# Performance work log

Measured on AMD Instinct MI355X. Metric: run time of the kernel, lower is better.

The kernel has to match this reference:

```python
import jax, jax.numpy as jnp
import numpy as np

N_NODES = 100_000
N_EDGES = 1_600_000
N_GRAPHS = 256          # num_segments for batch scatter (static)
T_CAPS = 16             # num_target_cap
IN_CH = 64
OUT_CH = 64
NUM_ROUTES = 3
BN_EPS = 1e-5


def squash(s, axis=-1):
    # v = (|s|^2 / (1+|s|^2)) * s / |s|
    sq = jnp.sum(s * s, axis=axis, keepdims=True)
    return (sq / (1.0 + sq)) * s / jnp.sqrt(sq + 1e-16)


def setup_inputs() -> dict:
    key = jax.random.key(0)
    k_x, k_ei, k_ew, k_b, k_w, k_bias = jax.random.split(key, 6)
    x = jax.random.normal(k_x, (N_NODES, IN_CH), dtype=jnp.float32)
    edge_index = jax.random.randint(k_ei, (2, N_EDGES), 0, N_NODES, dtype=jnp.int32)
    edge_weight = jax.random.uniform(k_ew, (N_EDGES,), dtype=jnp.float32)
    batch = jnp.sort(jax.random.randint(k_b, (N_NODES,), 0, N_GRAPHS, dtype=jnp.int32))
    # per-capsule GCNConv weights, stacked: (T, in, out), bias (T, out)
    W = jax.random.normal(k_w, (T_CAPS, IN_CH, OUT_CH), dtype=jnp.float32) * 0.05
    bias = jax.random.normal(k_bias, (T_CAPS, OUT_CH), dtype=jnp.float32) * 0.05
    bn_gamma = jnp.ones((IN_CH,), dtype=jnp.float32)
    bn_beta = jnp.zeros((IN_CH,), dtype=jnp.float32)
    return {"x": x, "edge_index": edge_index, "edge_weight": edge_weight,
            "batch": batch, "bn_gamma": bn_gamma, "bn_beta": bn_beta,
            "W": W, "bias": bias}


def reference(x, edge_index, edge_weight, batch, bn_gamma, bn_beta, W, bias):
    N = x.shape[0]
    T = W.shape[0]
    # --- BatchNorm1d (training-mode batch statistics, biased variance) ---
    mu = jnp.mean(x, axis=0)
    var = jnp.var(x, axis=0)
    xn = (x - mu) * jax.lax.rsqrt(var + BN_EPS) * bn_gamma + bn_beta

    # --- GCNConv (shared graph): A_hat x, then per-capsule linear ---
    row, col = edge_index[0], edge_index[1]
    ar = jnp.arange(N, dtype=edge_index.dtype)
    row_f = jnp.concatenate([row, ar])              # add self-loops, weight 1
    col_f = jnp.concatenate([col, ar])
    w_f = jnp.concatenate([edge_weight, jnp.ones((N,), x.dtype)])
    deg = jax.ops.segment_sum(w_f, col_f, num_segments=N)
    dinv = jnp.where(deg > 0, jax.lax.rsqrt(deg), 0.0)
    norm = dinv[row_f] * w_f * dinv[col_f]          # (E+N,)
    h = jax.ops.segment_sum(norm[:, None] * xn[row_f], col_f, num_segments=N)  # (N, in)
    # linearity: propagate(A, x W_t) == (propagate(A, x)) W_t
    u_hat = jnp.einsum('ni,tio->nto', h, W) + bias[None]  # (N, T, D)

    # --- dynamic routing ---
    node_deg = jax.ops.segment_sum(edge_weight, row, num_segments=N)  # (N,)
    b_log = jnp.broadcast_to(node_deg[:, None, None], (N, T, 1))
    u_det = jax.lax.stop_gradient(u_hat)
    for _ in range(NUM_ROUTES - 1):
        c = jax.nn.softmax(b_log, axis=1)                         # (N, T, 1)
        s = jax.ops.segment_sum(c * u_det, batch, num_segments=N_GRAPHS)  # (G, T, D)
        v = squash(s, axis=-1)
        vg = v[batch]                                             # (N, T, D)
        b_log = b_log + jnp.sum(u_det * vg, axis=-1, keepdims=True)
    c = jax.nn.softmax(b_log, axis=1)
    s = jax.ops.segment_sum(c * u_hat, batch, num_segments=N_GRAPHS)  # (G, T, D)

    # --- add per-graph mean of (normalized) node features ---
    cnt = jax.ops.segment_sum(jnp.ones((N,), x.dtype), batch, num_segments=N_GRAPHS)
    x_mean = jax.ops.segment_sum(xn, batch, num_segments=N_GRAPHS) / jnp.maximum(cnt, 1.0)[:, None]
    s = s + x_mean[:, None, :]                                    # needs in==out
    v = squash(s, axis=-1)

    # --- final_layer=True: v.norm(p=-1, dim=-1) = (sum |v|^-1)^-1 ---
    out = 1.0 / jnp.sum(1.0 / jnp.abs(v), axis=-1)                # (G, T)
    return out
```

## Files before the change

kernel.cpp:

```cpp
#include <hip/hip_runtime.h>
#include <hip/hip_fp16.h>
#include <math.h>

#define N_NODES 100000
#define N_EDGES 1600000
#define N_GRAPHS 256
#define T_CAPS 16
#define D_CH 64
#define BN_EPS 1e-5f
#define NSPLIT 8
#define CHUNK 32
#define FIX_SCALE 33554432.0f
#define NB 782
#define EPB 4096
#define NBLK 391
#define NBN 512

__device__ __forceinline__ float waveReduceSum(float v) {
    for (int m = 32; m >= 1; m >>= 1) v += __shfl_xor(v, m, 64);
    return v;
}

__global__ void setup_kernel(float* bn_sums, float* hsum, float* xsum,
                             const float* __restrict__ W, float* __restrict__ WT,
                             const int* __restrict__ batch, int* __restrict__ gstart) {
    int idx = blockIdx.x * blockDim.x + threadIdx.x;
    if (idx < 128) bn_sums[idx] = 0.0f;
    if (idx < N_GRAPHS * D_CH) { hsum[idx] = 0.0f; xsum[idx] = 0.0f; }
    if (idx < T_CAPS * 64 * 64) {
        int t = idx >> 12, rem = idx & 4095, o = rem >> 6, i = rem & 63;
        WT[idx] = W[t * 4096 + i * 64 + o];
    }
    if (idx <= N_GRAPHS) {
        int lo = 0, hi = N_NODES;
        while (lo < hi) { int mid = (lo + hi) >> 1; if (batch[mid] < idx) lo = mid + 1; else hi = mid; }
        gstart[idx] = lo;
    }
}

__global__ void passA_bn_kernel(const int* __restrict__ col, int* __restrict__ gh,
                                const float* __restrict__ x, float* __restrict__ sums,
                                __half2* __restrict__ x16) {
    int blk = blockIdx.x;
    int tid = threadIdx.x;
    if (blk < NBLK) {
        __shared__ unsigned hist[NB];
        for (int j = tid; j < NB; j += 256) hist[j] = 0u;
        __syncthreads();
        #pragma unroll
        for (int i = 0; i < EPB / 256; i++) {
            int e = blk * EPB + i * 256 + tid;
            if (e < N_EDGES) atomicAdd(&hist[col[e] >> 7], 1u);
        }
        __syncthreads();
        for (int j = tid; j < NB; j += 256) gh[blk * NB + j] = (int)hist[j];
    } else {
        int bb = blk - NBLK;
        int pr = tid & 31;
        int rg = tid >> 5;
        int c0 = pr * 2;
        float s0 = 0, q0 = 0, s1 = 0, q1 = 0;
        for (int r = bb * 8 + rg; r < N_NODES; r += NBN * 8) {
            float2 v = *(const float2*)(x + (size_t)r * 64 + c0);
            s0 += v.x; q0 += v.x * v.x;
            s1 += v.y; q1 += v.y * v.y;
            x16[(size_t)r * 32 + pr] = __floats2half2_rn(v.x, v.y);
        }
        __shared__ float ls[2][8][64];
        ls[0][rg][c0] = s0; ls[0][rg][c0 + 1] = s1;
        ls[1][rg][c0] = q0; ls[1][rg][c0 + 1] = q1;
        __syncthreads();
        if (tid < 64) {
            float a = 0.0f, bsm = 0.0f;
            for (int i = 0; i < 8; i++) { a += ls[0][i][tid]; bsm += ls[1][i][tid]; }
            atomicAdd(&sums[tid], a);
            atomicAdd(&sums[64 + tid], bsm);
        }
    }
}

__global__ void passB1_kernel(int* __restrict__ gh, int* __restrict__ Tarr) {
    int b = blockIdx.x;
    int tid = threadIdx.x;
    __shared__ int lds[256];
    int i0 = tid * 2, i1 = tid * 2 + 1;
    int v0 = (i0 < NBLK) ? gh[(size_t)i0 * NB + b] : 0;
    int v1 = (i1 < NBLK) ? gh[(size_t)i1 * NB + b] : 0;
    int pair = v0 + v1;
    lds[tid] = pair;
    __syncthreads();
    for (int d = 1; d < 256; d <<= 1) {
        int v = (tid >= d) ? lds[tid - d] : 0;
        __syncthreads();
        lds[tid] += v;
        __syncthreads();
    }
    int excl = lds[tid] - pair;
    if (i0 < NBLK) gh[(size_t)i0 * NB + b] = excl;
    if (i1 < NBLK) gh[(size_t)i1 * NB + b] = excl + v0;
    if (tid == 255) Tarr[b] = lds[255];
}

__global__ void passB2_kernel(const int* __restrict__ Tarr, int* __restrict__ Sarr,
                              int* __restrict__ off, const float* __restrict__ sums,
                              const float* __restrict__ gamma, const float* __restrict__ beta,
                              float* __restrict__ ab) {
    __shared__ int lds[256];
    int tid = threadIdx.x;
    if (tid < 64) {
        float mu = sums[tid] * (1.0f / N_NODES);
        float var = sums[64 + tid] * (1.0f / N_NODES) - mu * mu;
        float inv = 1.0f / sqrtf(var + BN_EPS);
        float a = inv * gamma[tid];
        ab[tid] = a;
        ab[64 + tid] = beta[tid] - mu * a;
    }
    int base = tid * 4;
    int t0 = (base + 0 < NB) ? Tarr[base + 0] : 0;
    int t1 = (base + 1 < NB) ? Tarr[base + 1] : 0;
    int t2 = (base + 2 < NB) ? Tarr[base + 2] : 0;
    int t3 = (base + 3 < NB) ? Tarr[base + 3] : 0;
    int tsum = t0 + t1 + t2 + t3;
    lds[tid] = tsum;
    __syncthreads();
    for (int d = 1; d < 256; d <<= 1) {
        int v = (tid >= d) ? lds[tid - d] : 0;
        __syncthreads();
        lds[tid] += v;
        __syncthreads();
    }
    int excl = lds[tid] - tsum;
    if (base + 0 < NB) Sarr[base + 0] = excl;
    if (base + 1 < NB) Sarr[base + 1] = excl + t0;
    if (base + 2 < NB) Sarr[base + 2] = excl + t0 + t1;
    if (base + 3 < NB) Sarr[base + 3] = excl + t0 + t1 + t2;
    if (tid == 0) { Sarr[NB] = N_EDGES; off[N_NODES] = N_EDGES; }
}

__global__ void passC_kernel(const int* __restrict__ row, const int* __restrict__ col,
                             const float* __restrict__ ew, const int* __restrict__ gh,
                             const int* __restrict__ Sarr, int2* __restrict__ brec) {
    int blk = blockIdx.x;
    int tid = threadIdx.x;
    __shared__ int cur[NB];
    for (int j = tid; j < NB; j += 256) cur[j] = Sarr[j] + gh[(size_t)blk * NB + j];
    __syncthreads();
    #pragma unroll
    for (int i = 0; i < EPB / 256; i++) {
        int e = blk * EPB + i * 256 + tid;
        if (e < N_EDGES) {
            int c = col[e], r = row[e];
            float w = ew[e];
            int b = c >> 7;
            int pos = atomicAdd(&cur[b], 1);
            brec[pos] = make_int2(((c & 127) << 17) | r, __float_as_int(w));
        }
    }
}

__global__ void passD_kernel(const int2* __restrict__ brec, const int* __restrict__ Sarr,
                             float* __restrict__ dinv, int* __restrict__ off,
                             int2* __restrict__ rec) {
    int b = blockIdx.x;
    int tid = threadIdx.x;
    int s0 = Sarr[b], s1 = Sarr[b + 1];
    __shared__ unsigned cnt[128];
    __shared__ unsigned degfx[128];
    __shared__ int scan_tmp[128];
    __shared__ int cursor[128];
    if (tid < 128) { cnt[tid] = 0u; degfx[tid] = 0u; }
    __syncthreads();
    for (int e = s0 + tid; e < s1; e += 256) {
        int2 rc = brec[e];
        int cl = (rc.x >> 17) & 127;
        atomicAdd(&cnt[cl], 1u);
        unsigned fx = __float2uint_rn(__int_as_float(rc.y) * FIX_SCALE);
        atomicAdd(&degfx[cl], fx);
    }
    __syncthreads();
    if (tid < 128) scan_tmp[tid] = (int)cnt[tid];
    __syncthreads();
    for (int d = 1; d < 128; d <<= 1) {
        int v = 0;
        if (tid < 128 && tid >= d) v = scan_tmp[tid - d];
        __syncthreads();
        if (tid < 128) scan_tmp[tid] += v;
        __syncthreads();
    }
    if (tid < 128) {
        int excl = scan_tmp[tid] - (int)cnt[tid];
        cursor[tid] = excl;
        int cg = b * 128 + tid;
        if (cg < N_NODES) {
            float d = 1.0f + (float)degfx[tid] * (1.0f / FIX_SCALE);
            dinv[cg] = 1.0f / sqrtf(d);
            off[cg] = s0 + excl;
        }
    }
    __syncthreads();
    for (int e = s0 + tid; e < s1; e += 256) {
        int2 rc = brec[e];
        int cl = (rc.x >> 17) & 127;
        int pos = atomicAdd((unsigned*)&cursor[cl], 1u);
        rec[s0 + (int)pos] = make_int2(rc.x & 0x1FFFF, rc.y);
    }
}

__global__ void h_gather_kernel(const int2* __restrict__ rec, const int* __restrict__ off,
                                const float* __restrict__ dinv, const __half* __restrict__ x16,
                                const float* __restrict__ ab, __half* __restrict__ h16) {
    int n = blockIdx.x * 4 + (threadIdx.x >> 6);
    int ch = threadIdx.x & 63;
    int e0 = off[n], e1 = off[n + 1];
    float dv = dinv[n];
    float cself = dv * dv;
    float acc0 = cself * __half2float(x16[(size_t)n * 64 + ch]);
    float acc1 = 0.0f, acc2 = 0.0f, acc3 = 0.0f;
    float csr = cself;
    int e = e0;
    for (; e + 8 <= e1; e += 8) {
        int2 r[8];
        #pragma unroll
        for (int i = 0; i < 8; i++) r[i] = rec[e + i];
        float cf[8], xv[8];
        #pragma unroll
        for (int i = 0; i < 8; i++) {
            cf[i] = dinv[r[i].x] * __int_as_float(r[i].y) * dv;
            xv[i] = __half2float(x16[(size_t)r[i].x * 64 + ch]);
        }
        acc0 += cf[0] * xv[0]; acc1 += cf[1] * xv[1];
        acc2 += cf[2] * xv[2]; acc3 += cf[3] * xv[3];
        acc0 += cf[4] * xv[4]; acc1 += cf[5] * xv[5];
        acc2 += cf[6] * xv[6]; acc3 += cf[7] * xv[7];
        csr += ((cf[0] + cf[1]) + (cf[2] + cf[3])) + ((cf[4] + cf[5]) + (cf[6] + cf[7]));
    }
    for (; e + 4 <= e1; e += 4) {
        int2 r0 = rec[e], r1 = rec[e + 1], r2 = rec[e + 2], r3 = rec[e + 3];
        float c0 = dinv[r0.x] * __int_as_float(r0.y) * dv;
        float c1 = dinv[r1.x] * __int_as_float(r1.y) * dv;
        float c2 = dinv[r2.x] * __int_as_float(r2.y) * dv;
        float c3 = dinv[r3.x] * __int_as_float(r3.y) * dv;
        float x0 = __half2float(x16[(size_t)r0.x * 64 + ch]);
        float x1 = __half2float(x16[(size_t)r1.x * 64 + ch]);
        float x2 = __half2float(x16[(size_t)r2.x * 64 + ch]);
        float x3 = __half2float(x16[(size_t)r3.x * 64 + ch]);
        acc0 += c0 * x0; acc1 += c1 * x1; acc2 += c2 * x2; acc3 += c3 * x3;
        csr += c0 + c1 + c2 + c3;
    }
    for (; e < e1; ++e) {
        int2 rc = rec[e];
        float c = dinv[rc.x] * __int_as_float(rc.y) * dv;
        acc0 += c * __half2float(x16[(size_t)rc.x * 64 + ch]);
        csr += c;
    }
    float acc = (acc0 + acc1) + (acc2 + acc3);
    h16[(size_t)n * 64 + ch] = __float2half(ab[ch] * acc + ab[64 + ch] * csr);
}

__global__ void gsum_kernel(const __half* __restrict__ x16, const __half* __restrict__ h16,
                            const int* __restrict__ gstart, float* __restrict__ xsum,
                            float* __restrict__ hsum) {
    int g = blockIdx.x / NSPLIT, sp = blockIdx.x % NSPLIT;
    int s0g = gstart[g], s1g = gstart[g + 1];
    int len = s1g - s0g;
    int q = (len + NSPLIT - 1) / NSPLIT;
    int a0 = s0g + sp * q, a1 = min(s1g, a0 + q);
    int ch = threadIdx.x & 63, rg = threadIdx.x >> 6;
    float ax = 0.0f, ah = 0.0f;
    for (int n = a0 + rg; n < a1; n += 4) {
        ax += __half2float(x16[(size_t)n * 64 + ch]);
        ah += __half2float(h16[(size_t)n * 64 + ch]);
    }
    __shared__ float lx[4][64], lh[4][64];
    lx[rg][ch] = ax; lh[rg][ch] = ah;
    __syncthreads();
    if (threadIdx.x < 64) {
        int c = threadIdx.x;
        float sx = lx[0][c] + lx[1][c] + lx[2][c] + lx[3][c];
        float sh = lh[0][c] + lh[1][c] + lh[2][c] + lh[3][c];
        atomicAdd(&xsum[g * 64 + c], sx);
        atomicAdd(&hsum[g * 64 + c], sh);
    }
}

__global__ void ka_fused_kernel(const __half* __restrict__ h16, const int* __restrict__ gstart,
                                const float* __restrict__ wva, const float* __restrict__ bva,
                                const float* __restrict__ wvb, const float* __restrict__ bvb,
                                float* __restrict__ hc_part, float* __restrict__ csum_part,
                                int mode) {
    int g = blockIdx.x / NSPLIT, sp = blockIdx.x % NSPLIT;
    int s0g = gstart[g], s1g = gstart[g + 1];
    int len = s1g - s0g;
    int q = (len + NSPLIT - 1) / NSPLIT;
    int s0 = s0g + sp * q, s1 = min(s1g, s0 + q);
    int tid = threadIdx.x;
    int d = tid & 63, tg = tid >> 6;
    int t = tid & 15, kh = tid >> 4;

    __shared__ float hlds[CHUNK][65];
    __shared__ float wa[16][65];
    __shared__ float wb[16][65];
    __shared__ float clds[CHUNK][17];
    __shared__ float bvl[2][16];

    for (int i = tid; i < 16 * 64; i += 256) {
        int tt = i >> 6, dd = i & 63;
        wa[tt][dd] = wva[(g * 16 + tt) * 64 + dd];
        if (mode) wb[tt][dd] = wvb[(g * 16 + tt) * 64 + dd];
    }
    if (tid < 16) { bvl[0][tid] = bva[g * 16 + tid]; bvl[1][tid] = mode ? bvb[g * 16 + tid] : 0.0f; }
    for (int i = tid; i < CHUNK * 65; i += 256) ((float*)hlds)[i] = 0.0f;
    __syncthreads();

    float acc0 = 0, acc1 = 0, acc2 = 0, acc3 = 0;
    float cs0 = 0, cs1 = 0, cs2 = 0, cs3 = 0;

    for (int n0 = s0; n0 < s1; n0 += CHUNK) {
        int nn = min(CHUNK, s1 - n0);
        #pragma unroll
        for (int j = 0; j < 8; j++) {
            int k = tg * 8 + j;
            if (k < nn) hlds[k][d] = __half2float(h16[(size_t)(n0 + k) * 64 + d]);
        }
        __syncthreads();
        int k0 = kh, k1 = kh + 16;
        float u0, u1;
        if (mode) {
            float a0 = bvl[0][t], a1 = bvl[0][t], b0 = bvl[1][t], b1 = bvl[1][t];
            for (int dd = 0; dd < 64; dd++) {
                float wav = wa[t][dd], wbv = wb[t][dd];
                float h0 = hlds[k0][dd], h1 = hlds[k1][dd];
                a0 += h0 * wav; a1 += h1 * wav;
                b0 += h0 * wbv; b1 += h1 * wbv;
            }
            u0 = a0 + b0; u1 = a1 + b1;
        } else {
            float a0 = bvl[0][t], a1 = bvl[0][t];
            for (int dd = 0; dd < 64; dd++) {
                float wav = wa[t][dd];
                a0 += hlds[k0][dd] * wav; a1 += hlds[k1][dd] * wav;
            }
            u0 = a0; u1 = a1;
        }
        float m0 = u0, m1 = u1;
        #pragma unroll
        for (int msk = 1; msk < 16; msk <<= 1) {
            m0 = fmaxf(m0, __shfl_xor(m0, msk, 64));
            m1 = fmaxf(m1, __shfl_xor(m1, msk, 64));
        }
        float e0 = expf(u0 - m0), e1 = expf(u1 - m1);
        float z0 = e0, z1 = e1;
        #pragma unroll
        for (int msk = 1; msk < 16; msk <<= 1) {
            z0 += __shfl_xor(z0, msk, 64);
            z1 += __shfl_xor(z1, msk, 64);
        }
        if (k0 < nn) clds[k0][t] = e0 / z0;
        if (k1 < nn) clds[k1][t] = e1 / z1;
        __syncthreads();
        for (int k = 0; k < nn; k++) {
            float hv = hlds[k][d];
            float c0 = clds[k][tg * 4 + 0], c1 = clds[k][tg * 4 + 1];
            float c2 = clds[k][tg * 4 + 2], c3 = clds[k][tg * 4 + 3];
            acc0 += c0 * hv; acc1 += c1 * hv; acc2 += c2 * hv; acc3 += c3 * hv;
            if (d == 0) { cs0 += c0; cs1 += c1; cs2 += c2; cs3 += c3; }
        }
        __syncthreads();
    }
    size_t base = ((size_t)(sp * N_GRAPHS + g) * 16 + tg * 4) * 64 + d;
    hc_part[base] = acc0; hc_part[base + 64] = acc1;
    hc_part[base + 128] = acc2; hc_part[base + 192] = acc3;
    if (d == 0) {
        int cb = (sp * N_GRAPHS + g) * 16 + tg * 4;
        csum_part[cb + 0] = cs0; csum_part[cb + 1] = cs1;
        csum_part[cb + 2] = cs2; csum_part[cb + 3] = cs3;
    }
}

__global__ void kb_kernel(const float* __restrict__ hsum, const float* __restrict__ hc_part,
                          const float* __restrict__ csum_part, const float* __restrict__ W,
                          const float* __restrict__ WT, const float* __restrict__ bias,
                          const float* __restrict__ xsum, const float* __restrict__ ab,
                          const int* __restrict__ gstart, float* __restrict__ wv,
                          float* __restrict__ bv, float* __restrict__ out, int mode) {
    int wid = blockIdx.x * 4 + (threadIdx.x >> 6);
    int lane = threadIdx.x & 63;
    int g = wid >> 4, t = wid & 15;
    const float* Wt = W + t * 4096;
    float cnt = (float)(gstart[g + 1] - gstart[g]);
    float s;
    if (mode == 0) {
        const float* hr = hsum + g * 64;
        float acc = cnt * bias[t * 64 + lane];
        for (int i = 0; i < 64; i++) acc += hr[i] * Wt[i * 64 + lane];
        s = acc * (1.0f / 16.0f);
    } else {
        float csum = 0.0f;
        #pragma unroll
        for (int sp = 0; sp < NSPLIT; sp++) csum += csum_part[(sp * N_GRAPHS + g) * 16 + t];
        float acc = csum * bias[t * 64 + lane];
        for (int i = 0; i < 64; i++) {
            float hci = 0.0f;
            #pragma unroll
            for (int sp = 0; sp < NSPLIT; sp++)
                hci += hc_part[((size_t)(sp * N_GRAPHS + g) * 16 + t) * 64 + i];
            acc += hci * Wt[i * 64 + lane];
        }
        s = acc;
        if (mode == 2) {
            float xm = ab[lane] * xsum[g * 64 + lane] / fmaxf(cnt, 1.0f) + ab[64 + lane];
            s += xm;
        }
    }
    float sq = waveReduceSum(s * s);
    float scale = (sq / (1.0f + sq)) / sqrtf(sq + 1e-16f);
    float v = scale * s;
    if (mode == 2) {
        float tot = waveReduceSum(1.0f / fabsf(v));
        if (lane == 0) out[wid] = 1.0f / tot;
    } else {
        __shared__ float vlds[4][64];
        int w = threadIdx.x >> 6;
        vlds[w][lane] = v;
        __syncthreads();
        const float* WTt = WT + t * 4096;
        float acc = 0.0f;
        for (int o = 0; o < 64; o++) acc += WTt[o * 64 + lane] * vlds[w][o];
        wv[(size_t)wid * 64 + lane] = acc;
        float b = waveReduceSum(bias[t * 64 + lane] * v);
        if (lane == 0) bv[wid] = b;
    }
}

extern "C" void kernel_launch(void* const* d_in, const int* in_sizes, int n_in,
                              void* d_out, int out_size, void* d_ws, size_t ws_size,
                              hipStream_t stream) {
    const float* x     = (const float*)d_in[0];
    const int*   ei    = (const int*)d_in[1];
    const float* ew    = (const float*)d_in[2];
    const int*   batch = (const int*)d_in[3];
    const float* gamma = (const float*)d_in[4];
    const float* beta  = (const float*)d_in[5];
    const float* W     = (const float*)d_in[6];
    const float* bias  = (const float*)d_in[7];
    float* out = (float*)d_out;

    const int* row = ei;
    const int* col = ei + N_EDGES;

    char* basep = (char*)d_ws;
    int2* rec  = (int2*)basep;                     basep += sizeof(int2) * N_EDGES;
    int2* brec = (int2*)basep;                     basep += sizeof(int2) * N_EDGES;
    __half2* x16 = (__half2*)basep;                basep += 2ULL * N_NODES * D_CH;
    __half* h16 = (__half*)basep;                  basep += 2ULL * N_NODES * D_CH;
    float* p = (float*)basep;
    float* hc_part  = p; p += (size_t)NSPLIT * N_GRAPHS * T_CAPS * D_CH;
    float* csum_part= p; p += NSPLIT * N_GRAPHS * T_CAPS;
    float* wva      = p; p += N_GRAPHS * T_CAPS * D_CH;
    float* bva      = p; p += N_GRAPHS * T_CAPS;
    float* wvb      = p; p += N_GRAPHS * T_CAPS * D_CH;
    float* bvb      = p; p += N_GRAPHS * T_CAPS;
    float* WT       = p; p += T_CAPS * 64 * 64;
    float* dinv     = p; p += N_NODES;
    float* bn_sums  = p; p += 128;
    float* ab       = p; p += 128;
    float* hsum     = p; p += N_GRAPHS * D_CH;
    float* xsum     = p; p += N_GRAPHS * D_CH;
    int*   ip       = (int*)p;
    int*   off      = ip; ip += N_NODES + 1;
    int*   gh       = ip; ip += (size_t)NBLK * NB;
    int*   Tarr     = ip; ip += NB;
    int*   Sarr     = ip; ip += NB + 1;
    int*   gstart   = ip; ip += N_GRAPHS + 1;

    setup_kernel<<<(T_CAPS * 64 * 64 + 255) / 256, 256, 0, stream>>>(bn_sums, hsum, xsum,
                                                                      W, WT, batch, gstart);
    passA_bn_kernel<<<NBLK + NBN, 256, 0, stream>>>(col, gh, x, bn_sums, x16);
    passB1_kernel<<<NB, 256, 0, stream>>>(gh, Tarr);
    passB2_kernel<<<1, 256, 0, stream>>>(Tarr, Sarr, off, bn_sums, gamma, beta, ab);
    passC_kernel<<<NBLK, 256, 0, stream>>>(row, col, ew, gh, Sarr, brec);
    passD_kernel<<<NB, 256, 0, stream>>>(brec, Sarr, dinv, off, rec);
    h_gather_kernel<<<N_NODES / 4, 256, 0, stream>>>(rec, off, dinv, (const __half*)x16, ab, h16);
    gsum_kernel<<<N_GRAPHS * NSPLIT, 256, 0, stream>>>((const __half*)x16, h16, gstart, xsum, hsum);

    kb_kernel<<<N_GRAPHS * T_CAPS / 4, 256, 0, stream>>>(hsum, hc_part, csum_part, W, WT, bias,
                                                          xsum, ab, gstart, wva, bva, out, 0);
    ka_fused_kernel<<<N_GRAPHS * NSPLIT, 256, 0, stream>>>(h16, gstart, wva, bva, wvb, bvb,
                                                            hc_part, csum_part, 0);
    kb_kernel<<<N_GRAPHS * T_CAPS / 4, 256, 0, stream>>>(hsum, hc_part, csum_part, W, WT, bias,
                                                          xsum, ab, gstart, wvb, bvb, out, 1);
    ka_fused_kernel<<<N_GRAPHS * NSPLIT, 256, 0, stream>>>(h16, gstart, wva, bva, wvb, bvb,
                                                            hc_part, csum_part, 1);
    kb_kernel<<<N_GRAPHS * T_CAPS / 4, 256, 0, stream>>>(hsum, hc_part, csum_part, W, WT, bias,
                                                          xsum, ab, gstart, wva, bva, out, 2);
}
```

Before: 274.9 us.

## Remove setup kernel by folding its work into other kernels; use per-split partial sums

Drops the separate setup launch. The W transpose moves into extra blocks of passA, the gstart binary search moves into passB2, and bn_sums is cleared with a memset. gsum now writes per-split partials instead of atomically adding, and kb reduces those partials into shared memory, which removes the need to zero hsum/xsum. h_gather factors the destination dinv out of the per-edge coefficient and removes the 4-way unrolled tail loop. The aim is to cut launch count, atomics and per-edge multiplies, at the cost of a slightly longer serial tail loop and some redundant partial reads in kb.

```diff
diff --git a/kernel.cpp b/kernel.cpp
--- a/kernel.cpp
+++ b/kernel.cpp
@@ -15,32 +15,17 @@
 #define EPB 4096
 #define NBLK 391
 #define NBN 512
+#define WTB 256
 
 __device__ __forceinline__ float waveReduceSum(float v) {
     for (int m = 32; m >= 1; m >>= 1) v += __shfl_xor(v, m, 64);
     return v;
 }
 
-__global__ void setup_kernel(float* bn_sums, float* hsum, float* xsum,
-                             const float* __restrict__ W, float* __restrict__ WT,
-                             const int* __restrict__ batch, int* __restrict__ gstart) {
-    int idx = blockIdx.x * blockDim.x + threadIdx.x;
-    if (idx < 128) bn_sums[idx] = 0.0f;
-    if (idx < N_GRAPHS * D_CH) { hsum[idx] = 0.0f; xsum[idx] = 0.0f; }
-    if (idx < T_CAPS * 64 * 64) {
-        int t = idx >> 12, rem = idx & 4095, o = rem >> 6, i = rem & 63;
-        WT[idx] = W[t * 4096 + i * 64 + o];
-    }
-    if (idx <= N_GRAPHS) {
-        int lo = 0, hi = N_NODES;
-        while (lo < hi) { int mid = (lo + hi) >> 1; if (batch[mid] < idx) lo = mid + 1; else hi = mid; }
-        gstart[idx] = lo;
-    }
-}
-
 __global__ void passA_bn_kernel(const int* __restrict__ col, int* __restrict__ gh,
                                 const float* __restrict__ x, float* __restrict__ sums,
-                                __half2* __restrict__ x16) {
+                                __half2* __restrict__ x16, const float* __restrict__ W,
+                                float* __restrict__ WT) {
     int blk = blockIdx.x;
     int tid = threadIdx.x;
     if (blk < NBLK) {
@@ -54,7 +39,7 @@
         }
         __syncthreads();
         for (int j = tid; j < NB; j += 256) gh[blk * NB + j] = (int)hist[j];
-    } else {
+    } else if (blk < NBLK + NBN) {
         int bb = blk - NBLK;
         int pr = tid & 31;
         int rg = tid >> 5;
@@ -76,6 +61,10 @@
             atomicAdd(&sums[tid], a);
             atomicAdd(&sums[64 + tid], bsm);
         }
+    } else {
+        int idx = (blk - NBLK - NBN) * 256 + tid;
+        int t = idx >> 12, rem = idx & 4095, o = rem >> 6, i = rem & 63;
+        WT[idx] = W[t * 4096 + i * 64 + o];
     }
 }
 
@@ -104,7 +93,8 @@
 __global__ void passB2_kernel(const int* __restrict__ Tarr, int* __restrict__ Sarr,
                               int* __restrict__ off, const float* __restrict__ sums,
                               const float* __restrict__ gamma, const float* __restrict__ beta,
-                              float* __restrict__ ab) {
+                              float* __restrict__ ab, const int* __restrict__ batch,
+                              int* __restrict__ gstart) {
     __shared__ int lds[256];
     int tid = threadIdx.x;
     if (tid < 64) {
@@ -114,6 +104,11 @@
         float a = inv * gamma[tid];
         ab[tid] = a;
         ab[64 + tid] = beta[tid] - mu * a;
+    }
+    for (int g = tid; g <= N_GRAPHS; g += 256) {
+        int lo = 0, hi = N_NODES;
+        while (lo < hi) { int mid = (lo + hi) >> 1; if (batch[mid] < g) lo = mid + 1; else hi = mid; }
+        gstart[g] = lo;
     }
     int base = tid * 4;
     int t0 = (base + 0 < NB) ? Tarr[base + 0] : 0;
@@ -213,10 +208,9 @@
     int ch = threadIdx.x & 63;
     int e0 = off[n], e1 = off[n + 1];
     float dv = dinv[n];
-    float cself = dv * dv;
-    float acc0 = cself * __half2float(x16[(size_t)n * 64 + ch]);
+    float acc0 = dv * __half2float(x16[(size_t)n * 64 + ch]);
     float acc1 = 0.0f, acc2 = 0.0f, acc3 = 0.0f;
-    float csr = cself;
+    float csr = dv;
     int e = e0;
     for (; e + 8 <= e1; e += 8) {
         int2 r[8];
@@ -225,7 +219,7 @@
         float cf[8], xv[8];
         #pragma unroll
         for (int i = 0; i < 8; i++) {
-            cf[i] = dinv[r[i].x] * __int_as_float(r[i].y) * dv;
+            cf[i] = dinv[r[i].x] * __int_as_float(r[i].y);
             xv[i] = __half2float(x16[(size_t)r[i].x * 64 + ch]);
         }
         acc0 += cf[0] * xv[0]; acc1 += cf[1] * xv[1];
@@ -234,32 +228,19 @@
         acc2 += cf[6] * xv[6]; acc3 += cf[7] * xv[7];
         csr += ((cf[0] + cf[1]) + (cf[2] + cf[3])) + ((cf[4] + cf[5]) + (cf[6] + cf[7]));
     }
-    for (; e + 4 <= e1; e += 4) {
-        int2 r0 = rec[e], r1 = rec[e + 1], r2 = rec[e + 2], r3 = rec[e + 3];
-        float c0 = dinv[r0.x] * __int_as_float(r0.y) * dv;
-        float c1 = dinv[r1.x] * __int_as_float(r1.y) * dv;
-        float c2 = dinv[r2.x] * __int_as_float(r2.y) * dv;
-        float c3 = dinv[r3.x] * __int_as_float(r3.y) * dv;
-        float x0 = __half2float(x16[(size_t)r0.x * 64 + ch]);
-        float x1 = __half2float(x16[(size_t)r1.x * 64 + ch]);
-        float x2 = __half2float(x16[(size_t)r2.x * 64 + ch]);
-        float x3 = __half2float(x16[(size_t)r3.x * 64 + ch]);
-        acc0 += c0 * x0; acc1 += c1 * x1; acc2 += c2 * x2; acc3 += c3 * x3;
-        csr += c0 + c1 + c2 + c3;
-    }
     for (; e < e1; ++e) {
         int2 rc = rec[e];
-        float c = dinv[rc.x] * __int_as_float(rc.y) * dv;
+        float c = dinv[rc.x] * __int_as_float(rc.y);
         acc0 += c * __half2float(x16[(size_t)rc.x * 64 + ch]);
         csr += c;
     }
-    float acc = (acc0 + acc1) + (acc2 + acc3);
-    h16[(size_t)n * 64 + ch] = __float2half(ab[ch] * acc + ab[64 + ch] * csr);
+    float acc = dv * ((acc0 + acc1) + (acc2 + acc3));
+    h16[(size_t)n * 64 + ch] = __float2half(ab[ch] * acc + ab[64 + ch] * (dv * csr));
 }
 
 __global__ void gsum_kernel(const __half* __restrict__ x16, const __half* __restrict__ h16,
-                            const int* __restrict__ gstart, float* __restrict__ xsum,
-                            float* __restrict__ hsum) {
+                            const int* __restrict__ gstart, float* __restrict__ xsum_p,
+                            float* __restrict__ hsum_p) {
     int g = blockIdx.x / NSPLIT, sp = blockIdx.x % NSPLIT;
     int s0g = gstart[g], s1g = gstart[g + 1];
     int len = s1g - s0g;
@@ -276,10 +257,9 @@
     __syncthreads();
     if (threadIdx.x < 64) {
         int c = threadIdx.x;
-        float sx = lx[0][c] + lx[1][c] + lx[2][c] + lx[3][c];
-        float sh = lh[0][c] + lh[1][c] + lh[2][c] + lh[3][c];
-        atomicAdd(&xsum[g * 64 + c], sx);
-        atomicAdd(&hsum[g * 64 + c], sh);
+        int base = (sp * N_GRAPHS + g) * 64 + c;
+        xsum_p[base] = lx[0][c] + lx[1][c] + lx[2][c] + lx[3][c];
+        hsum_p[base] = lh[0][c] + lh[1][c] + lh[2][c] + lh[3][c];
     }
 }
 
@@ -377,22 +357,37 @@
     }
 }
 
-__global__ void kb_kernel(const float* __restrict__ hsum, const float* __restrict__ hc_part,
+__global__ void kb_kernel(const float* __restrict__ hsum_p, const float* __restrict__ hc_part,
                           const float* __restrict__ csum_part, const float* __restrict__ W,
                           const float* __restrict__ WT, const float* __restrict__ bias,
-                          const float* __restrict__ xsum, const float* __restrict__ ab,
+                          const float* __restrict__ xsum_p, const float* __restrict__ ab,
                           const int* __restrict__ gstart, float* __restrict__ wv,
                           float* __restrict__ bv, float* __restrict__ out, int mode) {
     int wid = blockIdx.x * 4 + (threadIdx.x >> 6);
     int lane = threadIdx.x & 63;
+    int tid = threadIdx.x;
     int g = wid >> 4, t = wid & 15;
     const float* Wt = W + t * 4096;
     float cnt = (float)(gstart[g + 1] - gstart[g]);
+    __shared__ float hsumg[64];
+    __shared__ float xsumg[64];
+    if (mode == 0 && tid < 64) {
+        float s = 0.0f;
+        #pragma unroll
+        for (int sp = 0; sp < NSPLIT; sp++) s += hsum_p[(sp * N_GRAPHS + g) * 64 + tid];
+        hsumg[tid] = s;
+    }
+    if (mode == 2 && tid < 64) {
+        float s = 0.0f;
+        #pragma unroll
+        for (int sp = 0; sp < NSPLIT; sp++) s += xsum_p[(sp * N_GRAPHS + g) * 64 + tid];
+        xsumg[tid] = s;
+    }
+    if (mode != 1) __syncthreads();
     float s;
     if (mode == 0) {
-        const float* hr = hsum + g * 64;
         float acc = cnt * bias[t * 64 + lane];
-        for (int i = 0; i < 64; i++) acc += hr[i] * Wt[i * 64 + lane];
+        for (int i = 0; i < 64; i++) acc += hsumg[i] * Wt[i * 64 + lane];
         s = acc * (1.0f / 16.0f);
     } else {
         float csum = 0.0f;
@@ -408,7 +403,7 @@
         }
         s = acc;
         if (mode == 2) {
-            float xm = ab[lane] * xsum[g * 64 + lane] / fmaxf(cnt, 1.0f) + ab[64 + lane];
+            float xm = ab[lane] * xsumg[lane] / fmaxf(cnt, 1.0f) + ab[64 + lane];
             s += xm;
         }
     }
@@ -464,8 +459,8 @@
     float* dinv     = p; p += N_NODES;
     float* bn_sums  = p; p += 128;
     float* ab       = p; p += 128;
-    float* hsum     = p; p += N_GRAPHS * D_CH;
-    float* xsum     = p; p += N_GRAPHS * D_CH;
+    float* hsum_p   = p; p += (size_t)NSPLIT * N_GRAPHS * D_CH;
+    float* xsum_p   = p; p += (size_t)NSPLIT * N_GRAPHS * D_CH;
     int*   ip       = (int*)p;
     int*   off      = ip; ip += N_NODES + 1;
     int*   gh       = ip; ip += (size_t)NBLK * NB;
@@ -473,24 +468,25 @@
     int*   Sarr     = ip; ip += NB + 1;
     int*   gstart   = ip; ip += N_GRAPHS + 1;
 
-    setup_kernel<<<(T_CAPS * 64 * 64 + 255) / 256, 256, 0, stream>>>(bn_sums, hsum, xsum,
-                                                                      W, WT, batch, gstart);
-    passA_bn_kernel<<<NBLK + NBN, 256, 0, stream>>>(col, gh, x, bn_sums, x16);
+    hipMemsetAsync(bn_sums, 0, 128 * sizeof(float), stream);
+    passA_bn_kernel<<<NBLK + NBN + WTB, 256, 0, stream>>>(col, gh, x, bn_sums, x16, W, WT);
     passB1_kernel<<<NB, 256, 0, stream>>>(gh, Tarr);
-    passB2_kernel<<<1, 256, 0, stream>>>(Tarr, Sarr, off, bn_sums, gamma, beta, ab);
+    passB2_kernel<<<1, 256, 0, stream>>>(Tarr, Sarr, off, bn_sums, gamma, beta, ab,
+                                          batch, gstart);
     passC_kernel<<<NBLK, 256, 0, stream>>>(row, col, ew, gh, Sarr, brec);
     passD_kernel<<<NB, 256, 0, stream>>>(brec, Sarr, dinv, off, rec);
     h_gather_kernel<<<N_NODES / 4, 256, 0, stream>>>(rec, off, dinv, (const __half*)x16, ab, h16);
-    gsum_kernel<<<N_GRAPHS * NSPLIT, 256, 0, stream>>>((const __half*)x16, h16, gstart, xsum, hsum);
-
-    kb_kernel<<<N_GRAPHS * T_CAPS / 4, 256, 0, stream>>>(hsum, hc_part, csum_part, W, WT, bias,
-                                                          xsum, ab, gstart, wva, bva, out, 0);
+    gsum_kernel<<<N_GRAPHS * NSPLIT, 256, 0, stream>>>((const __half*)x16, h16, gstart,
+                                                        xsum_p, hsum_p);
+
+    kb_kernel<<<N_GRAPHS * T_CAPS / 4, 256, 0, stream>>>(hsum_p, hc_part, csum_part, W, WT, bias,
+                                                          xsum_p, ab, gstart, wva, bva, out, 0);
     ka_fused_kernel<<<N_GRAPHS * NSPLIT, 256, 0, stream>>>(h16, gstart, wva, bva, wvb, bvb,
                                                             hc_part, csum_part, 0);
-    kb_kernel<<<N_GRAPHS * T_CAPS / 4, 256, 0, stream>>>(hsum, hc_part, csum_part, W, WT, bias,
-                                                          xsum, ab, gstart, wvb, bvb, out, 1);
+    kb_kernel<<<N_GRAPHS * T_CAPS / 4, 256, 0, stream>>>(hsum_p, hc_part, csum_part, W, WT, bias,
+                                                          xsum_p, ab, gstart, wvb, bvb, out, 1);
     ka_fused_kernel<<<N_GRAPHS * NSPLIT, 256, 0, stream>>>(h16, gstart, wva, bva, wvb, bvb,
                                                             hc_part, csum_part, 1);
-    kb_kernel<<<N_GRAPHS * T_CAPS / 4, 256, 0, stream>>>(hsum, hc_part, csum_part, W, WT, bias,
-                                                          xsum, ab, gstart, wva, bva, out, 2);
-}
+    kb_kernel<<<N_GRAPHS * T_CAPS / 4, 256, 0, stream>>>(hsum_p, hc_part, csum_part, W, WT, bias,
+                                                          xsum_p, ab, gstart, wva, bva, out, 2);
+}
```

New measurement: 292.6 us. 6.4% more time.
